# Kernel optimization log

Measured on AMD Instinct MI355X. Metric: run time of the kernel, lower is better.

Reference implementation:

```python
import jax, jax.numpy as jnp
import numpy as np
import math

NHEAD = 8
NEG = -1e9  # stand-in for float('-inf') in the torch mask

def _layernorm(x, g, b):
    m = x.mean(-1, keepdims=True)
    v = ((x - m) ** 2).mean(-1, keepdims=True)
    return (x - m) / jnp.sqrt(v + 1e-5) * g + b

def setup_inputs() -> dict:
    key = jax.random.key(0)
    ks = jax.random.split(key, 8)
    B, S, D, E, F, L, C = 32, 512, 9, 256, 1024, 4, 10
    p = lambda k, shape: jax.random.normal(k, shape, dtype=jnp.float32) * 0.02
    return dict(
        src=jax.random.normal(ks[0], (B, S, D), dtype=jnp.float32),
        emb_W=p(ks[1], (E, D)), emb_b=jnp.zeros((E,), jnp.float32),
        Wqkv=p(ks[2], (L, 3 * E, E)), bqkv=jnp.zeros((L, 3 * E), jnp.float32),
        Wo=p(ks[3], (L, E, E)), bo=jnp.zeros((L, E), jnp.float32),
        ln1_g=jnp.ones((L, E), jnp.float32), ln1_b=jnp.zeros((L, E), jnp.float32),
        ln2_g=jnp.ones((L, E), jnp.float32), ln2_b=jnp.zeros((L, E), jnp.float32),
        W1=p(ks[4], (L, F, E)), b1=jnp.zeros((L, F), jnp.float32),
        W2=p(ks[5], (L, E, F)), b2=jnp.zeros((L, E), jnp.float32),
        dec_W=p(ks[6], (C, E)),
    )

def reference(src, emb_W, emb_b, Wqkv, bqkv, Wo, bo, ln1_g, ln1_b,
              ln2_g, ln2_b, W1, b1, W2, b2, dec_W):
    B, S, _ = src.shape
    E = emb_W.shape[0]
    H = NHEAD
    hd = E // H
    L = Wqkv.shape[0]

    # custom sparse mask: diagonal-only attention, except the last query row
    # attends to everything but itself (has_src_mask=True branch)
    eye = jnp.eye(S, dtype=src.dtype)
    mask = jnp.where(eye > 0, 0.0, NEG)
    mask = mask.at[-1, :].set(0.0).at[-1, -1].set(NEG)

    # sinusoidal positional encoding [S, E]
    pos = jnp.arange(S, dtype=jnp.float32)[:, None]
    div = jnp.exp(jnp.arange(0, E, 2, dtype=jnp.float32) * (-math.log(10000.0) / E))
    pe = jnp.zeros((S, E), jnp.float32)
    pe = pe.at[:, 0::2].set(jnp.sin(pos * div)).at[:, 1::2].set(jnp.cos(pos * div))

    # embed + scale + pos-enc (batch-first layout; math identical to seq-first)
    x = (src @ emb_W.T + emb_b) * math.sqrt(E) + pe[None, :, :]

    attns = []
    for l in range(L):  # small fixed number of layers
        qkv = x @ Wqkv[l].T + bqkv[l]  # [B,S,3E]
        q, k, v = jnp.split(qkv, 3, axis=-1)
        rs = lambda t: t.reshape(B, S, H, hd).transpose(0, 2, 1, 3)  # [B,H,S,hd]
        q, k, v = rs(q), rs(k), rs(v)
        scores = jnp.einsum('bhqd,bhkd->bhqk', q, k) / math.sqrt(hd) + mask
        a = jax.nn.softmax(scores, axis=-1)
        attns.append(a.mean(axis=1))  # head-averaged attention, as torch MHA returns
        o = jnp.einsum('bhqk,bhkd->bhqd', a, v).transpose(0, 2, 1, 3).reshape(B, S, E)
        x = _layernorm(x + (o @ Wo[l].T + bo[l]), ln1_g[l], ln1_b[l])
        f = jax.nn.relu(x @ W1[l].T + b1[l]) @ W2[l].T + b2[l]
        x = _layernorm(x + f, ln2_g[l], ln2_b[l])

    x = jax.nn.relu(x)
    out = (x @ dec_W.T).mean(axis=1)  # mean over sequence
    out = jax.nn.log_softmax(out, axis=-1)
    return out, jnp.stack(attns)
```

## Files before the change

### kernel.cpp

```cpp
#include <hip/hip_runtime.h>
#include <hip/hip_bf16.h>
#include <math.h>

namespace {

constexpr int BATCH = 32;
constexpr int SEQ   = 512;
constexpr int DIN   = 9;
constexpr int EMB   = 256;
constexpr int FF    = 1024;
constexpr int NLAYER= 4;
constexpr int NCLS  = 10;
constexpr int NHEADS= 8;
constexpr int HDIM  = 32;
constexpr int NTOK  = BATCH*SEQ;

typedef __attribute__((ext_vector_type(8))) short short8;
typedef __attribute__((ext_vector_type(4))) float floatx4;

#define GLOAD_LDS16(g, l) __builtin_amdgcn_global_load_lds( \
    (const __attribute__((address_space(1))) unsigned*)(g), \
    (__attribute__((address_space(3))) unsigned*)(l), 16, 0, 0)

#define WAITCNT(N) asm volatile("s_waitcnt vmcnt(" #N ")" ::: "memory")

template<bool RELU, bool KV>
__global__ __launch_bounds__(256)
void gemm_mfma(const __hip_bfloat16* __restrict__ A, int lda,
               const __hip_bfloat16* __restrict__ W,
               const float* __restrict__ bias,
               __hip_bfloat16* __restrict__ C0,
               __hip_bfloat16* __restrict__ C1,
               int ldc, int K)
{
    __shared__ __hip_bfloat16 As[2*128*32];
    __shared__ __hip_bfloat16 Bs[2*128*32];
    const int bm = blockIdx.y*128, bn = blockIdx.x*128;
    const int tid  = threadIdx.x;
    const int lane = tid & 63;
    const int w    = tid >> 6;
    const int wm   = (w >> 1)*64, wn = (w & 1)*64;

    floatx4 acc[4][4] = {};

    const int srow = w*32 + (lane >> 2);
    const int scol = (lane & 3)*8;
    const __hip_bfloat16* gA0 = A + (size_t)(bm + srow)*lda + scol;
    const __hip_bfloat16* gA1 = A + (size_t)(bm + srow + 16)*lda + scol;
    const __hip_bfloat16* gB0 = W + (size_t)(bn + srow)*K + scol;
    const __hip_bfloat16* gB1 = W + (size_t)(bn + srow + 16)*K + scol;
    const int l0 = (w*2)*512, l1 = (w*2 + 1)*512;

#define GM_STAGE(buf, k0) do { \
    GLOAD_LDS16(gA0 + (k0), As + (buf)*4096 + l0); \
    GLOAD_LDS16(gA1 + (k0), As + (buf)*4096 + l1); \
    GLOAD_LDS16(gB0 + (k0), Bs + (buf)*4096 + l0); \
    GLOAD_LDS16(gB1 + (k0), Bs + (buf)*4096 + l1); } while (0)

    const int arow = wm + (lane & 15);
    const int brow = wn + (lane & 15);
    const int kh   = lane >> 4;
    const int nt   = K >> 5;

    GM_STAGE(0, 0);
    for (int t = 0; t < nt; t++) {
        const int cur = t & 1;
        if (t + 1 < nt) {
            GM_STAGE(cur ^ 1, (t+1)*32);
            WAITCNT(4);
        } else {
            WAITCNT(0);
        }
        __builtin_amdgcn_s_barrier();
        const short8* Ab = (const short8*)(As + cur*4096);
        const short8* Bb = (const short8*)(Bs + cur*4096);
        short8 af[4], bf[4];
        #pragma unroll
        for (int m = 0; m < 4; m++) af[m] = Ab[(arow + m*16)*4 + kh];
        #pragma unroll
        for (int n = 0; n < 4; n++) bf[n] = Bb[(brow + n*16)*4 + kh];
        #pragma unroll
        for (int m = 0; m < 4; m++)
            #pragma unroll
            for (int n = 0; n < 4; n++)
                acc[m][n] = __builtin_amdgcn_mfma_f32_16x16x32_bf16(af[m], bf[n], acc[m][n], 0, 0, 0);
        __builtin_amdgcn_s_barrier();
    }
#undef GM_STAGE

    __hip_bfloat16* Cb;
    int cb;
    if (KV && bn >= 256) { Cb = C1; cb = bn - 256; }
    else                 { Cb = C0; cb = bn; }

    const int crow0 = bm + wm + (lane >> 4)*4;
    #pragma unroll
    for (int n = 0; n < 4; n++) {
        const int coln = wn + (lane & 15) + n*16;
        const float bv = bias[bn + coln];
        #pragma unroll
        for (int m = 0; m < 4; m++) {
            #pragma unroll
            for (int r = 0; r < 4; r++) {
                int row = crow0 + m*16 + r;
                float v = acc[m][n][r] + bv;
                if (RELU) v = fmaxf(v, 0.f);
                Cb[(size_t)row*ldc + cb + coln] = __float2bfloat16(v);
            }
        }
    }
}

__device__ __forceinline__ void stageB(const __hip_bfloat16* __restrict__ W, int ldw,
                                       int rowbase, int kbase,
                                       __hip_bfloat16* LB, int buf, int w, int lane)
{
    #pragma unroll
    for (int i = 0; i < 4; i++) {
        int rc = 4*w + i;
        const __hip_bfloat16* src = W + (size_t)(rowbase + rc*16 + (lane >> 2))*ldw
                                      + kbase + (lane & 3)*8;
        GLOAD_LDS16(src, LB + buf*8192 + rc*512);
    }
}

__device__ __forceinline__ void mfma8(const short8* Ab, const short8* Bb,
                                      floatx4* acc, int rgrp, int colhalf,
                                      int cl, int kh)
{
    short8 af = Ab[rgrp*64 + cl*4 + kh];
    #pragma unroll
    for (int n = 0; n < 8; n++) {
        short8 bf = Bb[(colhalf*8 + n)*64 + cl*4 + kh];
        acc[n] = __builtin_amdgcn_mfma_f32_16x16x32_bf16(af, bf, acc[n], 0, 0, 0);
    }
}

__global__ __launch_bounds__(256, 2)
void layer_tail(const __hip_bfloat16* __restrict__ vbuf,
                const __hip_bfloat16* __restrict__ obuf,
                const __hip_bfloat16* __restrict__ Wo,
                const float* __restrict__ bo,
                const float* __restrict__ g1, const float* __restrict__ b1ln,
                const __hip_bfloat16* __restrict__ W1,
                const float* __restrict__ b1f,
                const __hip_bfloat16* __restrict__ W2,
                const float* __restrict__ b2f,
                const float* __restrict__ g2, const float* __restrict__ b2ln,
                __hip_bfloat16* __restrict__ xb16)
{
    __shared__ __hip_bfloat16 SM[34816];
    __hip_bfloat16* LB = SM;
    __hip_bfloat16* LA = SM + 16384;
    __hip_bfloat16* X1 = SM + 18432;
    __hip_bfloat16* HC = SM + 26624;
    float* RED = (float*)LA;

    const int bm   = blockIdx.x*32;
    const int tid  = threadIdx.x;
    const int lane = tid & 63;
    const int w    = tid >> 6;
    const int rgrp = w & 1;
    const int colhalf = w >> 1;
    const int cl   = lane & 15;
    const int rg   = lane >> 4;
    const int kh   = lane >> 4;

    floatx4 acc[8] = {};
    const __hip_bfloat16* asrc = nullptr;
    if (w >= 2) {
        int a = w - 2;
        int grow = bm + a*16 + (lane >> 2);
        bool isl = (grow & (SEQ-1)) == (SEQ-1);
        asrc = (isl ? obuf + (size_t)(grow >> 9)*EMB
                    : vbuf + (size_t)grow*EMB) + (lane & 3)*8;
    }
    stageB(Wo, 256, 0, 0, LB, 0, w, lane);
    if (w >= 2) GLOAD_LDS16(asrc, LA + (w-2)*512);
    for (int t = 0; t < 8; t++) {
        const int cur = t & 1;
        if (t < 7) {
            stageB(Wo, 256, 0, (t+1)*32, LB, cur^1, w, lane);
            if (w >= 2) GLOAD_LDS16(asrc + (t+1)*32, LA + (cur^1)*1024 + (w-2)*512);
            WAITCNT(4);
        } else WAITCNT(0);
        __builtin_amdgcn_s_barrier();
        mfma8((const short8*)(LA + cur*1024), (const short8*)(LB + cur*8192),
              acc, rgrp, colhalf, cl, kh);
        __builtin_amdgcn_s_barrier();
    }
    {
        float gv[8], bbv[8], bv[8];
        #pragma unroll
        for (int n = 0; n < 8; n++) {
            int col = colhalf*128 + n*16 + cl;
            bv[n] = bo[col]; gv[n] = g1[col]; bbv[n] = b1ln[col];
        }
        #pragma unroll
        for (int r = 0; r < 4; r++) {
            int row = bm + rgrp*16 + rg*4 + r;
            const __hip_bfloat16* xr = xb16 + (size_t)row*EMB + colhalf*128;
            float S = 0.f, Q = 0.f;
            #pragma unroll
            for (int n = 0; n < 8; n++) {
                float v = acc[n][r] + bv[n] + __bfloat162float(xr[n*16 + cl]);
                acc[n][r] = v; S += v; Q += v*v;
            }
            #pragma unroll
            for (int o = 1; o < 16; o <<= 1) { S += __shfl_xor(S, o); Q += __shfl_xor(Q, o); }
            if (cl == 0) {
                int idx = rgrp*16 + rg*4 + r;
                RED[colhalf*32 + idx] = S;
                RED[64 + colhalf*32 + idx] = Q;
            }
        }
        __syncthreads();
        #pragma unroll
        for (int r = 0; r < 4; r++) {
            int idx = rgrp*16 + rg*4 + r;
            float S = RED[idx] + RED[32 + idx];
            float Q = RED[64 + idx] + RED[96 + idx];
            float mean = S * (1.f/EMB);
            float var  = Q * (1.f/EMB) - mean*mean;
            float rstd = 1.f / sqrtf(var + 1e-5f);
            #pragma unroll
            for (int n = 0; n < 8; n++) {
                int col = colhalf*128 + n*16 + cl;
                float v = (acc[n][r] - mean)*rstd*gv[n] + bbv[n];
                X1[(col >> 5)*1024 + rgrp*512 + (rg*4 + r)*32 + (col & 31)] = __float2bfloat16(v);
            }
        }
        __syncthreads();
    }

    floatx4 acc2[8] = {};
    for (int c = 0; c < 4; c++) {
        floatx4 fa[8] = {};
        stageB(W1, 256, c*256, 0, LB, 0, w, lane);
        for (int t = 0; t < 8; t++) {
            const int cur = t & 1;
            if (t < 7) { stageB(W1, 256, c*256, (t+1)*32, LB, cur^1, w, lane); WAITCNT(4); }
            else WAITCNT(0);
            __builtin_amdgcn_s_barrier();
            mfma8((const short8*)X1 + t*128, (const short8*)(LB + cur*8192),
                  fa, rgrp, colhalf, cl, kh);
            __builtin_amdgcn_s_barrier();
        }
        #pragma unroll
        for (int n = 0; n < 8; n++) {
            int colh = colhalf*128 + n*16 + cl;
            float bb = b1f[c*256 + colh];
            #pragma unroll
            for (int r = 0; r < 4; r++) {
                float v = fmaxf(fa[n][r] + bb, 0.f);
                HC[(colh >> 5)*1024 + rgrp*512 + (rg*4 + r)*32 + (colh & 31)] = __float2bfloat16(v);
            }
        }
        __syncthreads();
        stageB(W2, 1024, 0, c*256, LB, 0, w, lane);
        for (int t = 0; t < 8; t++) {
            const int cur = t & 1;
            if (t < 7) { stageB(W2, 1024, 0, c*256 + (t+1)*32, LB, cur^1, w, lane); WAITCNT(4); }
            else WAITCNT(0);
            __builtin_amdgcn_s_barrier();
            mfma8((const short8*)HC + t*128, (const short8*)(LB + cur*8192),
                  acc2, rgrp, colhalf, cl, kh);
            __builtin_amdgcn_s_barrier();
        }
    }

    {
        float gv[8], bbv[8], bv[8];
        #pragma unroll
        for (int n = 0; n < 8; n++) {
            int col = colhalf*128 + n*16 + cl;
            bv[n] = b2f[col]; gv[n] = g2[col]; bbv[n] = b2ln[col];
        }
        #pragma unroll
        for (int r = 0; r < 4; r++) {
            float S = 0.f, Q = 0.f;
            #pragma unroll
            for (int n = 0; n < 8; n++) {
                int col = colhalf*128 + n*16 + cl;
                float x1v = __bfloat162float(X1[(col >> 5)*1024 + rgrp*512 + (rg*4 + r)*32 + (col & 31)]);
                float v = acc2[n][r] + bv[n] + x1v;
                acc2[n][r] = v; S += v; Q += v*v;
            }
            #pragma unroll
            for (int o = 1; o < 16; o <<= 1) { S += __shfl_xor(S, o); Q += __shfl_xor(Q, o); }
            if (cl == 0) {
                int idx = rgrp*16 + rg*4 + r;
                RED[colhalf*32 + idx] = S;
                RED[64 + colhalf*32 + idx] = Q;
            }
        }
        __syncthreads();
        #pragma unroll
        for (int r = 0; r < 4; r++) {
            int idx = rgrp*16 + rg*4 + r;
            int row = bm + idx;
            float S = RED[idx] + RED[32 + idx];
            float Q = RED[64 + idx] + RED[96 + idx];
            float mean = S * (1.f/EMB);
            float var  = Q * (1.f/EMB) - mean*mean;
            float rstd = 1.f / sqrtf(var + 1e-5f);
            __hip_bfloat16* xr = xb16 + (size_t)row*EMB + colhalf*128;
            #pragma unroll
            for (int n = 0; n < 8; n++) {
                float v = (acc2[n][r] - mean)*rstd*gv[n] + bbv[n];
                xr[n*16 + cl] = __float2bfloat16(v);
            }
        }
    }
}

__global__ void f2b_all(const float* __restrict__ s0, const float* __restrict__ s1,
                        const float* __restrict__ s2, const float* __restrict__ s3,
                        __hip_bfloat16* __restrict__ d0, __hip_bfloat16* __restrict__ d1,
                        __hip_bfloat16* __restrict__ d2, __hip_bfloat16* __restrict__ d3)
{
    int blk = blockIdx.x;
    const float* s; __hip_bfloat16* d; int base;
    if      (blk <  768) { s = s0; d = d0; base = blk; }
    else if (blk < 1024) { s = s1; d = d1; base = blk - 768; }
    else if (blk < 2048) { s = s2; d = d2; base = blk - 1024; }
    else                 { s = s3; d = d3; base = blk - 2048; }
    int i = (base*256 + threadIdx.x)*4;
    float4 v = *(const float4*)(s + i);
    __hip_bfloat16 tmp[4];
    tmp[0] = __float2bfloat16(v.x); tmp[1] = __float2bfloat16(v.y);
    tmp[2] = __float2bfloat16(v.z); tmp[3] = __float2bfloat16(v.w);
    *(ushort4*)(d + i) = *(const ushort4*)tmp;
}

__global__ void embed_kernel(const float* __restrict__ src,
                             const float* __restrict__ emb_W,
                             const float* __restrict__ emb_b,
                             __hip_bfloat16* __restrict__ xb)
{
    int row = blockIdx.x;
    int e = threadIdx.x;
    int s = row % SEQ;
    const float* sr = src + (size_t)row*DIN;
    float acc = emb_b[e];
    #pragma unroll
    for (int d = 0; d < DIN; d++) acc += sr[d]*emb_W[e*DIN + d];
    acc *= 16.0f;
    int i2 = e & ~1;
    float div = expf(-(float)i2 * (9.210340371976184f / (float)EMB));
    float ang = (float)s * div;
    float pe = (e & 1) ? cosf(ang) : sinf(ang);
    xb[(size_t)row*EMB + e] = __float2bfloat16(acc + pe);
}

__global__ __launch_bounds__(512)
void attn_last_head(const __hip_bfloat16* __restrict__ xb,
                    const __hip_bfloat16* __restrict__ Wq,
                    const float* __restrict__ bq,
                    const __hip_bfloat16* __restrict__ kbuf,
                    const __hip_bfloat16* __restrict__ vbuf,
                    __hip_bfloat16* __restrict__ obuf,
                    float* __restrict__ amh)
{
    const int h = blockIdx.x, b = blockIdx.y;
    const int t = threadIdx.x;
    __shared__ float xlast[EMB];
    __shared__ float qpart[HDIM][17];
    __shared__ float qh[HDIM];
    __shared__ float sc[SEQ];
    __shared__ float red1[8], red2[8];
    __shared__ float opart[16][HDIM];

    if (t < EMB) xlast[t] = __bfloat162float(xb[((size_t)b*SEQ + SEQ-1)*EMB + t]);
    __syncthreads();

    {
        int d = t & 31, c = t >> 5;
        const __hip_bfloat16* wr = Wq + (size_t)(h*HDIM + d)*EMB + c*16;
        short8 w0 = *(const short8*)(wr);
        short8 w1 = *(const short8*)(wr + 8);
        float p = 0.f;
        #pragma unroll
        for (int j = 0; j < 8; j++)
            p += xlast[c*16 + j]*__bfloat162float(((const __hip_bfloat16*)&w0)[j]);
        #pragma unroll
        for (int j = 0; j < 8; j++)
            p += xlast[c*16 + 8 + j]*__bfloat162float(((const __hip_bfloat16*)&w1)[j]);
        qpart[d][c] = p;
    }
    __syncthreads();
    if (t < HDIM) {
        float qv = bq[h*HDIM + t];
        #pragma unroll
        for (int c = 0; c < 16; c++) qv += qpart[t][c];
        qh[t] = qv;
    }
    __syncthreads();

    {
        const __hip_bfloat16* krow = kbuf + ((size_t)b*SEQ + t)*EMB + h*HDIM;
        float s = 0.f;
        #pragma unroll
        for (int vv = 0; vv < 4; vv++) {
            short8 kk = *(const short8*)(krow + vv*8);
            #pragma unroll
            for (int j = 0; j < 8; j++)
                s += qh[vv*8 + j]*__bfloat162float(((const __hip_bfloat16*)&kk)[j]);
        }
        s *= 0.17677669529663687f;
        if (t == SEQ-1) s += -1e9f;
        sc[t] = s;
    }
    __syncthreads();

    {
        int wv = t >> 6, lane = t & 63;
        float m = sc[t];
        #pragma unroll
        for (int o = 32; o; o >>= 1) m = fmaxf(m, __shfl_xor(m, o));
        if (lane == 0) red1[wv] = m;
        __syncthreads();
        m = red1[0];
        #pragma unroll
        for (int i = 1; i < 8; i++) m = fmaxf(m, red1[i]);
        float e = expf(sc[t] - m);
        float s = e;
        #pragma unroll
        for (int o = 32; o; o >>= 1) s += __shfl_xor(s, o);
        if (lane == 0) red2[wv] = s;
        __syncthreads();
        float tot = red2[0]+red2[1]+red2[2]+red2[3]+red2[4]+red2[5]+red2[6]+red2[7];
        float a = e / tot;
        sc[t] = a;
        amh[((size_t)b*NHEADS + h)*SEQ + t] = a;
    }
    __syncthreads();

    {
        int e = t & 31, part = t >> 5;
        float o = 0.f;
        const __hip_bfloat16* vc = vbuf + (size_t)b*SEQ*EMB + h*HDIM + e;
        for (int k = part*32; k < part*32 + 32; k++)
            o += sc[k]*__bfloat162float(vc[(size_t)k*EMB]);
        opart[part][e] = o;
    }
    __syncthreads();
    if (t < HDIM) {
        float o = 0.f;
        #pragma unroll
        for (int p = 0; p < 16; p++) o += opart[p][t];
        obuf[b*EMB + h*HDIM + t] = __float2bfloat16(o);
    }
}

__global__ void write_attns(float* __restrict__ attns, const float* __restrict__ amh_all)
{
    constexpr int PER_ROW = SEQ/4;
    size_t tid = (size_t)blockIdx.x*blockDim.x + threadIdx.x;
    size_t row = tid / PER_ROW;
    int c4 = (int)(tid % PER_ROW);
    int q = (int)(row % SEQ);
    float4 v = make_float4(0.f,0.f,0.f,0.f);
    if (q == SEQ-1) {
        size_t lb = row / SEQ;
        const float* base = amh_all + lb*NHEADS*SEQ + c4*4;
        float x0=0.f, x1=0.f, x2=0.f, x3=0.f;
        #pragma unroll
        for (int h = 0; h < NHEADS; h++) {
            const float* r = base + (size_t)h*SEQ;
            x0 += r[0]; x1 += r[1]; x2 += r[2]; x3 += r[3];
        }
        v = make_float4(x0*0.125f, x1*0.125f, x2*0.125f, x3*0.125f);
    } else if ((q >> 2) == c4) {
        ((float*)&v)[q & 3] = 1.f;
    }
    ((float4*)attns)[tid] = v;
}

__global__ __launch_bounds__(512)
void decode_fused(const __hip_bfloat16* __restrict__ xb, const float* __restrict__ dec_W,
                  float* __restrict__ out)
{
    int b = blockIdx.x, t = threadIdx.x;
    int e = t & 255, half = t >> 8;
    __shared__ float rs[2][256];
    {
        const __hip_bfloat16* xp = xb + ((size_t)b*SEQ + half*256)*EMB + e;
        float r = 0.f;
        for (int i = 0; i < 256; i++) r += fmaxf(__bfloat162float(xp[(size_t)i*EMB]), 0.f);
        rs[half][e] = r;
    }
    __syncthreads();
    float part[NCLS];
    if (t < 256) {
        float rr = rs[0][t] + rs[1][t];
        #pragma unroll
        for (int c = 0; c < NCLS; c++) part[c] = rr * dec_W[c*EMB + t];
    } else {
        #pragma unroll
        for (int c = 0; c < NCLS; c++) part[c] = 0.f;
    }
    #pragma unroll
    for (int o = 32; o; o >>= 1)
        #pragma unroll
        for (int c = 0; c < NCLS; c++) part[c] += __shfl_xor(part[c], o);
    __shared__ float red[8][NCLS];
    int wv = t >> 6, lane = t & 63;
    if (lane == 0)
        #pragma unroll
        for (int c = 0; c < NCLS; c++) red[wv][c] = part[c];
    __syncthreads();
    if (t == 0) {
        float lg[NCLS];
        float m = -1e30f;
        #pragma unroll
        for (int c = 0; c < NCLS; c++) {
            float s = 0.f;
            #pragma unroll
            for (int wvi = 0; wvi < 8; wvi++) s += red[wvi][c];
            lg[c] = s * (1.f/(float)SEQ);
            m = fmaxf(m, lg[c]);
        }
        float s = 0.f;
        #pragma unroll
        for (int c = 0; c < NCLS; c++) s += expf(lg[c] - m);
        float ls = logf(s);
        #pragma unroll
        for (int c = 0; c < NCLS; c++) out[b*NCLS + c] = lg[c] - m - ls;
    }
}

}

extern "C" void kernel_launch(void* const* d_in, const int* in_sizes, int n_in,
                              void* d_out, int out_size, void* d_ws, size_t ws_size,
                              hipStream_t stream)
{
    const float* src   = (const float*)d_in[0];
    const float* emb_W = (const float*)d_in[1];
    const float* emb_b = (const float*)d_in[2];
    const float* Wqkv  = (const float*)d_in[3];
    const float* bqkv  = (const float*)d_in[4];
    const float* Wo    = (const float*)d_in[5];
    const float* bo    = (const float*)d_in[6];
    const float* ln1_g = (const float*)d_in[7];
    const float* ln1_b = (const float*)d_in[8];
    const float* ln2_g = (const float*)d_in[9];
    const float* ln2_b = (const float*)d_in[10];
    const float* W1    = (const float*)d_in[11];
    const float* b1    = (const float*)d_in[12];
    const float* W2    = (const float*)d_in[13];
    const float* b2    = (const float*)d_in[14];
    const float* dec_W = (const float*)d_in[15];

    float* out   = (float*)d_out;
    float* attns = out + BATCH*NCLS;

    char* ws = (char*)d_ws;
    __hip_bfloat16* xb16 = (__hip_bfloat16*)ws;     ws += (size_t)NTOK*EMB*2;
    __hip_bfloat16* kbuf = (__hip_bfloat16*)ws;     ws += (size_t)NTOK*EMB*2;
    __hip_bfloat16* vbuf = (__hip_bfloat16*)ws;     ws += (size_t)NTOK*EMB*2;
    __hip_bfloat16* obuf = (__hip_bfloat16*)ws;     ws += (size_t)BATCH*EMB*2;
    __hip_bfloat16* wq16 = (__hip_bfloat16*)ws;     ws += (size_t)NLAYER*3*EMB*EMB*2;
    __hip_bfloat16* wo16 = (__hip_bfloat16*)ws;     ws += (size_t)NLAYER*EMB*EMB*2;
    __hip_bfloat16* w116 = (__hip_bfloat16*)ws;     ws += (size_t)NLAYER*FF*EMB*2;
    __hip_bfloat16* w216 = (__hip_bfloat16*)ws;     ws += (size_t)NLAYER*EMB*FF*2;
    float*          amall= (float*)ws;              ws += (size_t)NLAYER*BATCH*NHEADS*SEQ*4;

    f2b_all<<<3072, 256, 0, stream>>>(Wqkv, Wo, W1, W2, wq16, wo16, w116, w216);

    embed_kernel<<<NTOK, EMB, 0, stream>>>(src, emb_W, emb_b, xb16);

    for (int l = 0; l < NLAYER; l++) {
        const __hip_bfloat16* wql = wq16 + (size_t)l*3*EMB*EMB;
        const float* bql = bqkv + (size_t)l*3*EMB;

        gemm_mfma<false, true><<<dim3(512/128, NTOK/128), 256, 0, stream>>>(
            xb16, EMB, wql + (size_t)EMB*EMB, bql + EMB, kbuf, vbuf, EMB, EMB);

        attn_last_head<<<dim3(NHEADS, BATCH), 512, 0, stream>>>(
            xb16, wql, bql, kbuf, vbuf, obuf, amall + (size_t)l*BATCH*NHEADS*SEQ);

        layer_tail<<<NTOK/32, 256, 0, stream>>>(
            vbuf, obuf,
            wo16 + (size_t)l*EMB*EMB, bo + (size_t)l*EMB,
            ln1_g + l*EMB, ln1_b + l*EMB,
            w116 + (size_t)l*FF*EMB, b1 + (size_t)l*FF,
            w216 + (size_t)l*EMB*FF, b2 + (size_t)l*EMB,
            ln2_g + l*EMB, ln2_b + l*EMB,
            xb16);
    }

    {
        size_t total_f4 = (size_t)NLAYER*BATCH*SEQ*(SEQ/4);
        int blocks = (int)((total_f4 + 255)/256);
        write_attns<<<blocks, 256, 0, stream>>>(attns, amall);
    }

    decode_fused<<<BATCH, 512, 0, stream>>>(xb16, dec_W, out);
}
```

Before: 486.2 us.

## Fuse next-layer K/V projection into layer_tail epilogue

Moves the K/V projection for layer l+1 into the tail kernel of layer l. The freshly normalized rows are kept in shared memory and multiplied by the next layer's Wk/Wv, so the separate GEMM launch and its reread of the activations from global memory go away for layers 1-3. The cost is that layer_tail does more serial work per block, and correctness depends on the HC shared-memory layout matching what mfma8 expects. The tail also overwrites vbuf while it is being read, which is only safe if each block touches only its own rows.

```diff
diff --git a/kernel.cpp b/kernel.cpp
--- a/kernel.cpp
+++ b/kernel.cpp
@@ -147,7 +147,12 @@
                 const __hip_bfloat16* __restrict__ W2,
                 const float* __restrict__ b2f,
                 const float* __restrict__ g2, const float* __restrict__ b2ln,
-                __hip_bfloat16* __restrict__ xb16)
+                __hip_bfloat16* __restrict__ xb16,
+                const __hip_bfloat16* __restrict__ Wkv,
+                const float* __restrict__ bk,
+                const float* __restrict__ bv2,
+                __hip_bfloat16* __restrict__ kout,
+                __hip_bfloat16* __restrict__ vout)
 {
     __shared__ __hip_bfloat16 SM[34816];
     __hip_bfloat16* LB = SM;
@@ -307,8 +312,41 @@
             __hip_bfloat16* xr = xb16 + (size_t)row*EMB + colhalf*128;
             #pragma unroll
             for (int n = 0; n < 8; n++) {
+                int col = colhalf*128 + n*16 + cl;
                 float v = (acc2[n][r] - mean)*rstd*gv[n] + bbv[n];
-                xr[n*16 + cl] = __float2bfloat16(v);
+                __hip_bfloat16 hv = __float2bfloat16(v);
+                xr[n*16 + cl] = hv;
+                HC[(col >> 5)*1024 + rgrp*512 + (rg*4 + r)*32 + (col & 31)] = hv;
+            }
+        }
+    }
+
+    if (Wkv != nullptr) {
+        __syncthreads();
+        #pragma unroll
+        for (int nh = 0; nh < 2; nh++) {
+            floatx4 a3[8] = {};
+            const float* bkv = (nh == 0) ? bk : bv2;
+            __hip_bfloat16* dst = (nh == 0) ? kout : vout;
+            stageB(Wkv, 256, nh*256, 0, LB, 0, w, lane);
+            for (int t = 0; t < 8; t++) {
+                const int cur = t & 1;
+                if (t < 7) { stageB(Wkv, 256, nh*256, (t+1)*32, LB, cur^1, w, lane); WAITCNT(4); }
+                else WAITCNT(0);
+                __builtin_amdgcn_s_barrier();
+                mfma8((const short8*)HC + t*128, (const short8*)(LB + cur*8192),
+                      a3, rgrp, colhalf, cl, kh);
+                __builtin_amdgcn_s_barrier();
+            }
+            #pragma unroll
+            for (int n = 0; n < 8; n++) {
+                int col = colhalf*128 + n*16 + cl;
+                float bb = bkv[col];
+                #pragma unroll
+                for (int r = 0; r < 4; r++) {
+                    int row = bm + rgrp*16 + rg*4 + r;
+                    dst[(size_t)row*EMB + col] = __float2bfloat16(a3[n][r] + bb);
+                }
             }
         }
     }
@@ -571,16 +609,21 @@
 
     embed_kernel<<<NTOK, EMB, 0, stream>>>(src, emb_W, emb_b, xb16);
 
+    gemm_mfma<false, true><<<dim3(512/128, NTOK/128), 256, 0, stream>>>(
+        xb16, EMB, wq16 + (size_t)EMB*EMB, bqkv + EMB, kbuf, vbuf, EMB, EMB);
+
     for (int l = 0; l < NLAYER; l++) {
         const __hip_bfloat16* wql = wq16 + (size_t)l*3*EMB*EMB;
         const float* bql = bqkv + (size_t)l*3*EMB;
 
-        gemm_mfma<false, true><<<dim3(512/128, NTOK/128), 256, 0, stream>>>(
-            xb16, EMB, wql + (size_t)EMB*EMB, bql + EMB, kbuf, vbuf, EMB, EMB);
-
         attn_last_head<<<dim3(NHEADS, BATCH), 512, 0, stream>>>(
             xb16, wql, bql, kbuf, vbuf, obuf, amall + (size_t)l*BATCH*NHEADS*SEQ);
 
+        const bool last = (l == NLAYER-1);
+        const __hip_bfloat16* wkv_next = last ? nullptr
+            : wq16 + (size_t)(l+1)*3*EMB*EMB + (size_t)EMB*EMB;
+        const float* bk_next = last ? nullptr : bqkv + (size_t)(l+1)*3*EMB + EMB;
+        const float* bv_next = last ? nullptr : bqkv + (size_t)(l+1)*3*EMB + 2*EMB;
         layer_tail<<<NTOK/32, 256, 0, stream>>>(
             vbuf, obuf,
             wo16 + (size_t)l*EMB*EMB, bo + (size_t)l*EMB,
@@ -588,7 +631,9 @@
             w116 + (size_t)l*FF*EMB, b1 + (size_t)l*FF,
             w216 + (size_t)l*EMB*FF, b2 + (size_t)l*EMB,
             ln2_g + l*EMB, ln2_b + l*EMB,
-            xb16);
+            xb16,
+            wkv_next, bk_next, bv_next,
+            last ? nullptr : kbuf, last ? nullptr : vbuf);
     }
 
     {
```

Measured after the change: 481.4 us. Within noise of the previous version (-1.0%).
